# Performance work log

Hardware: AMD Instinct MI355X
Metric: run time of the kernel (lower is better)

## Reference

```python
import jax, jax.numpy as jnp
import numpy as np

SEQ = 4096
EMBED = 1280
HEADS = 16
HEAD_DIM = EMBED // HEADS  # 80


def rotate_half(x):
    # interleaved rotate: out[..., 2i] = -x[..., 2i+1]; out[..., 2i+1] = x[..., 2i]
    x_even = x[..., ::2]
    x_odd = x[..., 1::2]
    return jnp.stack((-x_odd, x_even), axis=-1).reshape(x.shape)


def setup_inputs() -> dict:
    key = jax.random.key(0)
    ks = jax.random.split(key, 7)
    return {
        "hidden_states": jax.random.normal(ks[0], (SEQ, EMBED), dtype=jnp.float32),
        "cos": jax.random.uniform(ks[1], (SEQ, HEAD_DIM), dtype=jnp.float32),
        "sin": jax.random.uniform(ks[2], (SEQ, HEAD_DIM), dtype=jnp.float32),
        "w_qkv": jax.random.normal(ks[3], (EMBED, 3 * EMBED), dtype=jnp.float32) * 0.02,
        "b_qkv": jax.random.normal(ks[4], (3 * EMBED,), dtype=jnp.float32) * 0.02,
        "w_proj": jax.random.normal(ks[5], (EMBED, EMBED), dtype=jnp.float32) * 0.02,
        "b_proj": jax.random.normal(ks[6], (EMBED,), dtype=jnp.float32) * 0.02,
    }


def reference(hidden_states, cos, sin, w_qkv, b_qkv, w_proj, b_proj):
    S = hidden_states.shape[0]
    # QKV projection: (S, 3E) -> (S, 3, H, D)
    qkv = (hidden_states @ w_qkv + b_qkv).reshape(S, 3, HEADS, HEAD_DIM)
    q, k, v = qkv[:, 0], qkv[:, 1], qkv[:, 2]  # each (S, H, D)

    # RoPE in float32, cos/sin broadcast over heads: (S, 1, D)
    dt = q.dtype
    qf, kf = q.astype(jnp.float32), k.astype(jnp.float32)
    c = cos[:, None, :].astype(jnp.float32)
    s = sin[:, None, :].astype(jnp.float32)
    q = (qf * c + rotate_half(qf) * s).astype(dt)
    k = (kf * c + rotate_half(kf) * s).astype(dt)

    scaling = HEAD_DIM ** -0.5
    # attention scores per head: (H, S, S)
    scores = jnp.einsum("shd,thd->hst", q, k) * scaling
    attn = jax.nn.softmax(scores.astype(jnp.float32), axis=-1).astype(dt)
    # weighted values: (S, H, D)
    out = jnp.einsum("hst,thd->shd", attn, v).reshape(S, EMBED)
    return out @ w_proj + b_proj
```

## Files before the change

### kernel.cpp

```cpp
#include <hip/hip_runtime.h>
#include <hip/hip_bf16.h>

#define SEQ   4096
#define EMBED 1280
#define NH    16
#define HD    80
#define K1    EMBED
#define N1    (3*EMBED)

typedef short bfrag_t __attribute__((ext_vector_type(8)));
typedef float f32x4   __attribute__((ext_vector_type(4)));
typedef float f32x16  __attribute__((ext_vector_type(16)));

static __device__ __forceinline__ unsigned short f2bf(float x){
    __hip_bfloat16 h = __float2bfloat16(x);
    return __builtin_bit_cast(unsigned short, h);
}
static __device__ __forceinline__ float bf2f(unsigned short u){
    unsigned int v = ((unsigned int)u) << 16;
    return __builtin_bit_cast(float, v);
}

static __device__ __forceinline__ unsigned int pack2bf(float a, float b){
    unsigned int ua = __builtin_bit_cast(unsigned int, a) + 0x8000u;
    unsigned int ub = __builtin_bit_cast(unsigned int, b) + 0x8000u;
#if __has_builtin(__builtin_amdgcn_perm)
    return __builtin_amdgcn_perm(ub, ua, 0x07060302u);
#else
    return (ua >> 16) | (ub & 0xFFFF0000u);
#endif
}

static __device__ __forceinline__ float fast_exp2(float x){
#if __has_builtin(__builtin_amdgcn_exp2f)
    return __builtin_amdgcn_exp2f(x);
#else
    return __expf(x * 0.69314718056f);
#endif
}

static __device__ __forceinline__ void gload_lds16(const void* g, void* l){
#if __has_builtin(__builtin_amdgcn_global_load_lds)
    __builtin_amdgcn_global_load_lds(
        (const __attribute__((address_space(1))) unsigned int*)g,
        (__attribute__((address_space(3))) unsigned int*)l, 16, 0, 0);
#else
    *(uint4*)l = *(const uint4*)g;
#endif
}


__global__ __launch_bounds__(256) void f32_to_bf16_k(const float* __restrict__ in,
                                                     unsigned short* __restrict__ out){
    int i = blockIdx.x * 256 + threadIdx.x;
    float4 v = ((const float4*)in)[i];
    ushort4 r;
    r.x = f2bf(v.x); r.y = f2bf(v.y); r.z = f2bf(v.z); r.w = f2bf(v.w);
    ((ushort4*)out)[i] = r;
}

__global__ __launch_bounds__(256) void transpose_to_bf16(const float* __restrict__ in,
                                                         unsigned short* __restrict__ out,
                                                         int R, int C){
    __shared__ float t[32][33];
    int bc = blockIdx.x * 32, br = blockIdx.y * 32;
    int tx = threadIdx.x & 31, ty = threadIdx.x >> 5;
    for (int i = ty; i < 32; i += 8) t[i][tx] = in[(size_t)(br + i) * C + bc + tx];
    __syncthreads();
    for (int i = ty; i < 32; i += 8) out[(size_t)(bc + i) * R + br + tx] = f2bf(t[tx][i]);
}


template<int EPI>
__global__ __launch_bounds__(256)
void gemm128(const unsigned short* __restrict__ A,
             const unsigned short* __restrict__ BT,
             const float* __restrict__ bias,
             const float* __restrict__ cosp, const float* __restrict__ sinp,
             unsigned short* __restrict__ qout, unsigned short* __restrict__ kout,
             unsigned short* __restrict__ vout,
             float* __restrict__ out,
             int M, int N, int K)
{
    __shared__ union {
        struct { unsigned short A[128*32]; unsigned short B[128*32]; } ab;
        unsigned short tr[4][64][72];
    } lds;

    int tid  = threadIdx.x;
    int lane = tid & 63, wave = tid >> 6;
    int wm = wave >> 1, wn = wave & 1;
    int quad = lane >> 4, l16 = lane & 15;
    int m0 = blockIdx.y * 128, n0 = blockIdx.x * 128;

    f32x4 acc[4][4] = {};
    const unsigned short* ga = A  + (size_t)(m0 + (tid>>2)) * K + (tid&3)*8;
    const unsigned short* gb = BT + (size_t)(n0 + (tid>>2)) * K + (tid&3)*8;

    for (int k0 = 0; k0 < K; k0 += 32){
        __syncthreads();
        gload_lds16(ga,                &lds.ab.A[tid*8]);
        gload_lds16(ga + (size_t)64*K, &lds.ab.A[2048 + tid*8]);
        gload_lds16(gb,                &lds.ab.B[tid*8]);
        gload_lds16(gb + (size_t)64*K, &lds.ab.B[2048 + tid*8]);
        ga += 32; gb += 32;
        __syncthreads();
        bfrag_t af[4], bf[4];
        #pragma unroll
        for (int i = 0; i < 4; i++)
            af[i] = *(const bfrag_t*)&lds.ab.A[(wm*64 + i*16 + l16)*32 + quad*8];
        #pragma unroll
        for (int j = 0; j < 4; j++)
            bf[j] = *(const bfrag_t*)&lds.ab.B[(wn*64 + j*16 + l16)*32 + quad*8];
        #pragma unroll
        for (int i = 0; i < 4; i++)
            #pragma unroll
            for (int j = 0; j < 4; j++)
                acc[i][j] = __builtin_amdgcn_mfma_f32_16x16x32_bf16(af[i], bf[j], acc[i][j], 0, 0, 0);
    }

    const float scaling = 0.11180339887498949f;

    if (EPI == 0 && n0 >= 2*EMBED){
        __syncthreads();
        #pragma unroll
        for (int j = 0; j < 4; j++){
            int colw = j*16 + l16;
            float b = bias[n0 + wn*64 + colw];
            #pragma unroll
            for (int i = 0; i < 4; i++){
                ushort4 u;
                u.x = f2bf(acc[i][j][0] + b);
                u.y = f2bf(acc[i][j][1] + b);
                u.z = f2bf(acc[i][j][2] + b);
                u.w = f2bf(acc[i][j][3] + b);
                *(ushort4*)&lds.tr[wave][colw][i*16 + quad*4] = u;
            }
        }
        int c8 = lane >> 3, rc = lane & 7;
        #pragma unroll
        for (int cg = 0; cg < 8; cg++){
            int colw = cg*8 + c8;
            size_t colg = (size_t)(n0 - 2*EMBED) + wn*64 + colw;
            int rowg = m0 + wm*64 + rc*8;
            *(uint4*)&vout[colg*SEQ + rowg] = *(const uint4*)&lds.tr[wave][colw][rc*8];
        }
        return;
    }

    #pragma unroll
    for (int i = 0; i < 4; i++)
    #pragma unroll
    for (int j = 0; j < 4; j++){
        int col = n0 + wn*64 + j*16 + l16;
        float b = bias[col];
        #pragma unroll
        for (int r = 0; r < 4; r++){
            int row = m0 + wm*64 + i*16 + quad*4 + r;
            float v = acc[i][j][r] + b;
            if (EPI == 0){
                int which = col / EMBED;
                int rem   = col % EMBED;
                int h = rem / HD, d = rem % HD;
                float vo = __shfl_xor(v, 1, 64);
                float c = cosp[(size_t)row*HD + d];
                float s = sinp[(size_t)row*HD + d];
                float o = (d & 1) ? (v*c + vo*s) : (v*c - vo*s);
                if (which == 0)
                    qout[((size_t)h*SEQ + row)*HD + d] = f2bf(o * scaling);
                else
                    kout[((size_t)h*SEQ + row)*HD + d] = f2bf(o);
            } else {
                out[(size_t)row * N + col] = v;
            }
        }
    }
}


__global__ __launch_bounds__(256, 4)
void attn_mfma(const unsigned short* __restrict__ q,
               const unsigned short* __restrict__ k,
               const unsigned short* __restrict__ vt,
               unsigned short* __restrict__ out,
               unsigned short* __restrict__ opart,
               float* __restrict__ lpart,
               int iters)
{
    __shared__ unsigned short Vt[2][80*64];
    __shared__ unsigned short Ps[128][72];

    int tid  = threadIdx.x;
    int lane = tid & 63, wave = tid >> 6;
    int quad = lane >> 4, l16 = lane & 15;
    int l32  = lane & 31, h2 = lane >> 5;
    int h = blockIdx.y, q0 = blockIdx.x * 128;
    int split = blockIdx.z;
    int kb0 = split * iters * 64;
    int qrow = wave*32 + l32;

    const unsigned short* qh = q  + ((size_t)h*SEQ + q0)*HD;
    const unsigned short* kh = k  + (size_t)h*SEQ*HD;
    const unsigned short* vh = vt + (size_t)h*HD*SEQ;

    bfrag_t qf[5];
    #pragma unroll
    for (int kk = 0; kk < 5; kk++)
        qf[kk] = *(const bfrag_t*)&qh[(size_t)qrow*HD + (kk*2 + h2)*8];

    auto stage = [&](int buf, int kb){
        unsigned short* dst = &Vt[buf][0];
        #pragma unroll
        for (int rnd = 0; rnd < 3; rnd++){
            int idx = rnd*256 + tid;
            if (rnd < 2 || tid < 128){
                int row = idx >> 3, c = idx & 7;
                gload_lds16(&vh[(size_t)row*SEQ + kb + ((c ^ (row & 7)) << 3)], &dst[idx*8]);
            }
        }
    };

    stage(0, kb0);

    float la = 0.f, lb = 0.f;
    f32x4 o_[2][5] = {};

    const unsigned short* kp0 = kh + (size_t)(kb0 + l32)*HD + h2*8;
    const unsigned short* kp1 = kp0 + (size_t)32*HD;
    const float LOG2E = 1.44269504f;
    const float BIAS2 = -17.3123405f;

    for (int kt = 0; kt < iters; kt++){
        f32x16 S0 = {}, S1 = {};
        #pragma unroll
        for (int kk = 0; kk < 5; kk++){
            bfrag_t kf0 = *(const bfrag_t*)(kp0 + kk*16);
            bfrag_t kf1 = *(const bfrag_t*)(kp1 + kk*16);
            S0 = __builtin_amdgcn_mfma_f32_32x32x16_bf16(kf0, qf[kk], S0, 0,0,0);
            S1 = __builtin_amdgcn_mfma_f32_32x32x16_bf16(kf1, qf[kk], S1, 0,0,0);
        }
        kp0 += (size_t)64*HD; kp1 += (size_t)64*HD;

        #pragma unroll
        for (int r = 0; r < 16; r++){
            float p0 = fast_exp2(fmaf(S0[r], LOG2E, BIAS2));
            float p1 = fast_exp2(fmaf(S1[r], LOG2E, BIAS2));
            S0[r] = p0; S1[r] = p1;
            la += p0; lb += p1;
        }

        unsigned int* prow = (unsigned int*)&Ps[qrow][h2*4];
        #pragma unroll
        for (int g = 0; g < 4; g++){
            uint2 w0, w1;
            w0.x = pack2bf(S0[g*4+0], S0[g*4+1]);
            w0.y = pack2bf(S0[g*4+2], S0[g*4+3]);
            w1.x = pack2bf(S1[g*4+0], S1[g*4+1]);
            w1.y = pack2bf(S1[g*4+2], S1[g*4+3]);
            *(uint2*)&prow[g*4]      = w0;
            *(uint2*)&prow[16 + g*4] = w1;
        }

        __syncthreads();
        if (kt < iters - 1) stage((kt+1)&1, kb0 + (kt+1)*64);

        int buf = kt & 1;
        #pragma unroll
        for (int kk = 0; kk < 2; kk++){
            bfrag_t pf0 = *(const bfrag_t*)&Ps[wave*32      + l16][(kk*4+quad)*8];
            bfrag_t pf1 = *(const bfrag_t*)&Ps[wave*32 + 16 + l16][(kk*4+quad)*8];
            #pragma unroll
            for (int dt = 0; dt < 5; dt++){
                int row = dt*16 + l16;
                bfrag_t vf = *(const bfrag_t*)&Vt[buf][row*64 + (((kk*4+quad) ^ (l16 & 7)) << 3)];
                o_[0][dt] = __builtin_amdgcn_mfma_f32_16x16x32_bf16(vf, pf0, o_[0][dt], 0,0,0);
                o_[1][dt] = __builtin_amdgcn_mfma_f32_16x16x32_bf16(vf, pf1, o_[1][dt], 0,0,0);
            }
        }
    }

    float l_ = la + lb;
    l_ += __shfl_xor(l_, 32, 64);

    if (gridDim.z == 1){
        #pragma unroll
        for (int i = 0; i < 2; i++){
            float linv = 1.f / __shfl(l_, i*16 + l16, 64);
            int qg = q0 + wave*32 + i*16 + l16;
            #pragma unroll
            for (int dt = 0; dt < 5; dt++){
                int d = dt*16 + quad*4;
                ushort4 u;
                u.x = f2bf(o_[i][dt][0]*linv);
                u.y = f2bf(o_[i][dt][1]*linv);
                u.z = f2bf(o_[i][dt][2]*linv);
                u.w = f2bf(o_[i][dt][3]*linv);
                *(ushort4*)&out[(size_t)qg*EMBED + h*HD + d] = u;
            }
        }
    } else {
        if (h2 == 0)
            lpart[((size_t)(split*NH + h))*SEQ + q0 + qrow] = l_;
        #pragma unroll
        for (int i = 0; i < 2; i++){
            int qg = q0 + wave*32 + i*16 + l16;
            size_t base = (((size_t)(split*NH + h))*SEQ + qg)*HD;
            #pragma unroll
            for (int dt = 0; dt < 5; dt++){
                int d = dt*16 + quad*4;
                ushort4 u;
                u.x = f2bf(o_[i][dt][0]);
                u.y = f2bf(o_[i][dt][1]);
                u.z = f2bf(o_[i][dt][2]);
                u.w = f2bf(o_[i][dt][3]);
                *(ushort4*)&opart[base + d] = u;
            }
        }
    }
}

__global__ __launch_bounds__(256)
void attn_combine(const unsigned short* __restrict__ op,
                  const float* __restrict__ lp,
                  unsigned short* __restrict__ out)
{
    int t = blockIdx.x*256 + threadIdx.x;
    int d8 = t % 10;
    int qh = t / 10;
    int q  = qh & (SEQ-1);
    int h  = qh >> 12;
    size_t b0 = (((size_t)h*SEQ) + q)*HD + d8*8;
    size_t b1 = (((size_t)(NH + h)*SEQ) + q)*HD + d8*8;
    float inv = 1.f / (lp[(size_t)h*SEQ + q] + lp[(size_t)(NH + h)*SEQ + q]);
    uint4 A = *(const uint4*)&op[b0];
    uint4 B = *(const uint4*)&op[b1];
    uint4 R;
    unsigned int* a = (unsigned int*)&A;
    unsigned int* b = (unsigned int*)&B;
    unsigned int* r = (unsigned int*)&R;
    #pragma unroll
    for (int e = 0; e < 4; e++){
        float lo = (bf2f((unsigned short)(a[e] & 0xffff)) + bf2f((unsigned short)(b[e] & 0xffff))) * inv;
        float hi = (bf2f((unsigned short)(a[e] >> 16))    + bf2f((unsigned short)(b[e] >> 16)))    * inv;
        r[e] = pack2bf(lo, hi);
    }
    *(uint4*)&out[(size_t)q*EMBED + h*HD + d8*8] = R;
}


extern "C" void kernel_launch(void* const* d_in, const int* in_sizes, int n_in,
                              void* d_out, int out_size, void* d_ws, size_t ws_size,
                              hipStream_t stream)
{
    const float* hs    = (const float*)d_in[0];
    const float* cosp  = (const float*)d_in[1];
    const float* sinp  = (const float*)d_in[2];
    const float* wqkv  = (const float*)d_in[3];
    const float* bqkv  = (const float*)d_in[4];
    const float* wproj = (const float*)d_in[5];
    const float* bproj = (const float*)d_in[6];
    float* out = (float*)d_out;

    char* ws = (char*)d_ws;
    size_t off = 0;
    auto alloc = [&](size_t bytes){ void* p = ws + off; off += bytes; return p; };
    unsigned short* hb    = (unsigned short*)alloc((size_t)SEQ*EMBED*2);
    unsigned short* wqT   = (unsigned short*)alloc((size_t)N1*K1*2);
    unsigned short* wpT   = (unsigned short*)alloc((size_t)EMBED*EMBED*2);
    unsigned short* q_ws  = (unsigned short*)alloc((size_t)SEQ*EMBED*2);
    unsigned short* k_ws  = (unsigned short*)alloc((size_t)SEQ*EMBED*2);
    unsigned short* v_ws  = (unsigned short*)alloc((size_t)SEQ*EMBED*2);
    unsigned short* a_ws  = (unsigned short*)alloc((size_t)SEQ*EMBED*2);
    unsigned short* opart = (unsigned short*)alloc((size_t)2*NH*SEQ*HD*2);
    float*          lpart = (float*)alloc((size_t)2*NH*SEQ*4);
    int nsplit = (ws_size >= off) ? 2 : 1;

    f32_to_bf16_k<<<SEQ*EMBED/4/256, 256, 0, stream>>>(hs, hb);
    transpose_to_bf16<<<dim3(N1/32,    K1/32),    256, 0, stream>>>(wqkv,  wqT, K1,    N1);
    transpose_to_bf16<<<dim3(EMBED/32, EMBED/32), 256, 0, stream>>>(wproj, wpT, EMBED, EMBED);

    gemm128<0><<<dim3(N1/128, SEQ/128), 256, 0, stream>>>(
        hb, wqT, bqkv, cosp, sinp, q_ws, k_ws, v_ws, nullptr, SEQ, N1, K1);

    attn_mfma<<<dim3(SEQ/128, NH, nsplit), 256, 0, stream>>>(
        q_ws, k_ws, v_ws, a_ws, opart, lpart, (SEQ/64)/nsplit);
    if (nsplit == 2)
        attn_combine<<<NH*SEQ*10/256, 256, 0, stream>>>(opart, lpart, a_ws);

    gemm128<1><<<dim3(EMBED/128, SEQ/128), 256, 0, stream>>>(
        a_ws, wpT, bproj, nullptr, nullptr, nullptr, nullptr, nullptr, out, SEQ, EMBED, EMBED);
}
```

Baseline: 337.6 us.

## Prefetch K fragments into registers and restage RoPE epilogue through LDS

The attention loop now loads the next tile's K fragments into registers while the current QK^T MFMAs and softmax run. The V tile staging moves to the end of each iteration behind a single barrier at the top, instead of a mid-loop barrier. The P scratch buffer is repadded to 68 columns and read with two 8-byte loads per fragment. The QKV GEMM RoPE epilogue writes float results into an LDS tile, then emits coalesced 4-element bf16 stores instead of scattered 2-byte stores. The K prefetch raises register pressure, which may hurt occupancy at the 4-blocks-per-SIMD launch bound.

```diff
diff --git a/kernel.cpp b/kernel.cpp
--- a/kernel.cpp
+++ b/kernel.cpp
@@ -47,6 +47,13 @@
 #else
     *(uint4*)l = *(const uint4*)g;
 #endif
+}
+
+static __device__ __forceinline__ bfrag_t ld_frag8(const unsigned short* p){
+    uint2 lo = *(const uint2*)p;
+    uint2 hi = *(const uint2*)(p + 4);
+    uint4 u; u.x = lo.x; u.y = lo.y; u.z = hi.x; u.w = hi.y;
+    return __builtin_bit_cast(bfrag_t, u);
 }
 
 
@@ -85,6 +92,7 @@
     __shared__ union {
         struct { unsigned short A[128*32]; unsigned short B[128*32]; } ab;
         unsigned short tr[4][64][72];
+        float trf[4][16][68];
     } lds;
 
     int tid  = threadIdx.x;
@@ -148,6 +156,47 @@
         return;
     }
 
+    if (EPI == 0){
+        bool isq = (n0 < EMBED);
+        unsigned short* dst = isq ? qout : kout;
+        float mult = isq ? scaling : 1.f;
+        int colbase = (n0 - (isq ? 0 : EMBED)) + wn*64;
+        __syncthreads();
+        int rw = lane >> 2, cc = lane & 3;
+        #pragma unroll
+        for (int i = 0; i < 4; i++){
+            #pragma unroll
+            for (int j = 0; j < 4; j++){
+                int colw = j*16 + l16;
+                int col  = colbase + colw;
+                int d    = col % HD;
+                float b  = bias[n0 + wn*64 + colw];
+                #pragma unroll
+                for (int r = 0; r < 4; r++){
+                    int row = m0 + wm*64 + i*16 + quad*4 + r;
+                    float v = acc[i][j][r] + b;
+                    float vo = __shfl_xor(v, 1, 64);
+                    float c = cosp[(size_t)row*HD + d];
+                    float s = sinp[(size_t)row*HD + d];
+                    float o = (d & 1) ? (v*c + vo*s) : (v*c - vo*s);
+                    lds.trf[wave][quad*4 + r][colw] = o * mult;
+                }
+            }
+            #pragma unroll
+            for (int rnd = 0; rnd < 4; rnd++){
+                int colw = rnd*16 + cc*4;
+                float4 fv = *(const float4*)&lds.trf[wave][rw][colw];
+                int col = colbase + colw;
+                int hh = col / HD, d = col - hh*HD;
+                int rowg = m0 + wm*64 + i*16 + rw;
+                ushort4 u;
+                u.x = f2bf(fv.x); u.y = f2bf(fv.y); u.z = f2bf(fv.z); u.w = f2bf(fv.w);
+                *(ushort4*)&dst[((size_t)hh*SEQ + rowg)*HD + d] = u;
+            }
+        }
+        return;
+    }
+
     #pragma unroll
     for (int i = 0; i < 4; i++)
     #pragma unroll
@@ -157,22 +206,7 @@
         #pragma unroll
         for (int r = 0; r < 4; r++){
             int row = m0 + wm*64 + i*16 + quad*4 + r;
-            float v = acc[i][j][r] + b;
-            if (EPI == 0){
-                int which = col / EMBED;
-                int rem   = col % EMBED;
-                int h = rem / HD, d = rem % HD;
-                float vo = __shfl_xor(v, 1, 64);
-                float c = cosp[(size_t)row*HD + d];
-                float s = sinp[(size_t)row*HD + d];
-                float o = (d & 1) ? (v*c + vo*s) : (v*c - vo*s);
-                if (which == 0)
-                    qout[((size_t)h*SEQ + row)*HD + d] = f2bf(o * scaling);
-                else
-                    kout[((size_t)h*SEQ + row)*HD + d] = f2bf(o);
-            } else {
-                out[(size_t)row * N + col] = v;
-            }
+            out[(size_t)row * N + col] = acc[i][j][r] + b;
         }
     }
 }
@@ -188,7 +222,7 @@
                int iters)
 {
     __shared__ unsigned short Vt[2][80*64];
-    __shared__ unsigned short Ps[128][72];
+    __shared__ unsigned short Ps[128][68];
 
     int tid  = threadIdx.x;
     int lane = tid & 63, wave = tid >> 6;
@@ -225,21 +259,36 @@
     float la = 0.f, lb = 0.f;
     f32x4 o_[2][5] = {};
 
-    const unsigned short* kp0 = kh + (size_t)(kb0 + l32)*HD + h2*8;
-    const unsigned short* kp1 = kp0 + (size_t)32*HD;
+    const unsigned short* kp = kh + (size_t)(kb0 + l32)*HD + h2*8;
     const float LOG2E = 1.44269504f;
     const float BIAS2 = -17.3123405f;
 
+    bfrag_t kf[10];
+    #pragma unroll
+    for (int kk = 0; kk < 5; kk++){
+        kf[kk]   = *(const bfrag_t*)(kp + kk*16);
+        kf[5+kk] = *(const bfrag_t*)(kp + (size_t)32*HD + kk*16);
+    }
+    kp += (size_t)64*HD;
+
     for (int kt = 0; kt < iters; kt++){
+        __syncthreads();
+
         f32x16 S0 = {}, S1 = {};
         #pragma unroll
         for (int kk = 0; kk < 5; kk++){
-            bfrag_t kf0 = *(const bfrag_t*)(kp0 + kk*16);
-            bfrag_t kf1 = *(const bfrag_t*)(kp1 + kk*16);
-            S0 = __builtin_amdgcn_mfma_f32_32x32x16_bf16(kf0, qf[kk], S0, 0,0,0);
-            S1 = __builtin_amdgcn_mfma_f32_32x32x16_bf16(kf1, qf[kk], S1, 0,0,0);
-        }
-        kp0 += (size_t)64*HD; kp1 += (size_t)64*HD;
+            S0 = __builtin_amdgcn_mfma_f32_32x32x16_bf16(kf[kk],   qf[kk], S0, 0,0,0);
+            S1 = __builtin_amdgcn_mfma_f32_32x32x16_bf16(kf[5+kk], qf[kk], S1, 0,0,0);
+        }
+
+        if (kt + 1 < iters){
+            #pragma unroll
+            for (int kk = 0; kk < 5; kk++){
+                kf[kk]   = *(const bfrag_t*)(kp + kk*16);
+                kf[5+kk] = *(const bfrag_t*)(kp + (size_t)32*HD + kk*16);
+            }
+            kp += (size_t)64*HD;
+        }
 
         #pragma unroll
         for (int r = 0; r < 16; r++){
@@ -249,7 +298,6 @@
             la += p0; lb += p1;
         }
 
-        unsigned int* prow = (unsigned int*)&Ps[qrow][h2*4];
         #pragma unroll
         for (int g = 0; g < 4; g++){
             uint2 w0, w1;
@@ -257,18 +305,15 @@
             w0.y = pack2bf(S0[g*4+2], S0[g*4+3]);
             w1.x = pack2bf(S1[g*4+0], S1[g*4+1]);
             w1.y = pack2bf(S1[g*4+2], S1[g*4+3]);
-            *(uint2*)&prow[g*4]      = w0;
-            *(uint2*)&prow[16 + g*4] = w1;
-        }
-
-        __syncthreads();
-        if (kt < iters - 1) stage((kt+1)&1, kb0 + (kt+1)*64);
+            *(uint2*)&Ps[qrow][g*8 + h2*4]      = w0;
+            *(uint2*)&Ps[qrow][32 + g*8 + h2*4] = w1;
+        }
 
         int buf = kt & 1;
         #pragma unroll
         for (int kk = 0; kk < 2; kk++){
-            bfrag_t pf0 = *(const bfrag_t*)&Ps[wave*32      + l16][(kk*4+quad)*8];
-            bfrag_t pf1 = *(const bfrag_t*)&Ps[wave*32 + 16 + l16][(kk*4+quad)*8];
+            bfrag_t pf0 = ld_frag8(&Ps[wave*32      + l16][kk*32 + quad*8]);
+            bfrag_t pf1 = ld_frag8(&Ps[wave*32 + 16 + l16][kk*32 + quad*8]);
             #pragma unroll
             for (int dt = 0; dt < 5; dt++){
                 int row = dt*16 + l16;
@@ -277,6 +322,8 @@
                 o_[1][dt] = __builtin_amdgcn_mfma_f32_16x16x32_bf16(vf, pf1, o_[1][dt], 0,0,0);
             }
         }
+
+        if (kt + 1 < iters) stage((kt+1)&1, kb0 + (kt+1)*64);
     }
 
     float l_ = la + lb;
```

Measured after the change: 1.031 ms. +205.3%, slower.

## Software-pipeline attention loop: defer PV to next iteration, prefetch K, repack P tile

Applied to the files above, without the earlier changes.

Restructures the attention main loop so the P·V MFMAs for tile kt-1 run at the top of iteration kt, interleaved with the K fragment loads for tile kt. The single barrier now precedes the QK^T of the current tile instead of sitting between P writes and PV reads, and the final PV is done after the loop. K fragments are loaded in full register arrays ahead of use, and the P scratch row stride drops from 72 to 68 with a reordered column layout, read back with two 8-byte loads. The aim is to hide global and LDS latency and cut bank conflicts, at the cost of more live registers and possible occupancy pressure.

```diff
diff --git a/kernel.cpp b/kernel.cpp
--- a/kernel.cpp
+++ b/kernel.cpp
@@ -47,6 +47,13 @@
 #else
     *(uint4*)l = *(const uint4*)g;
 #endif
+}
+
+static __device__ __forceinline__ bfrag_t ld_frag8(const unsigned short* p){
+    uint2 lo = *(const uint2*)p;
+    uint2 hi = *(const uint2*)(p + 4);
+    uint4 u; u.x = lo.x; u.y = lo.y; u.z = hi.x; u.w = hi.y;
+    return __builtin_bit_cast(bfrag_t, u);
 }
 
 
@@ -188,7 +195,7 @@
                int iters)
 {
     __shared__ unsigned short Vt[2][80*64];
-    __shared__ unsigned short Ps[128][72];
+    __shared__ unsigned short Ps[128][68];
 
     int tid  = threadIdx.x;
     int lane = tid & 63, wave = tid >> 6;
@@ -220,26 +227,59 @@
         }
     };
 
+    auto pv = [&](int buf, f32x4 (&o_)[2][5]){
+        #pragma unroll
+        for (int kk = 0; kk < 2; kk++){
+            bfrag_t pf0 = ld_frag8(&Ps[wave*32      + l16][kk*32 + quad*8]);
+            bfrag_t pf1 = ld_frag8(&Ps[wave*32 + 16 + l16][kk*32 + quad*8]);
+            #pragma unroll
+            for (int dt = 0; dt < 5; dt++){
+                int row = dt*16 + l16;
+                bfrag_t vf = *(const bfrag_t*)&Vt[buf][row*64 + (((kk*4+quad) ^ (l16 & 7)) << 3)];
+                o_[0][dt] = __builtin_amdgcn_mfma_f32_16x16x32_bf16(vf, pf0, o_[0][dt], 0,0,0);
+                o_[1][dt] = __builtin_amdgcn_mfma_f32_16x16x32_bf16(vf, pf1, o_[1][dt], 0,0,0);
+            }
+        }
+    };
+
     stage(0, kb0);
 
     float la = 0.f, lb = 0.f;
     f32x4 o_[2][5] = {};
 
-    const unsigned short* kp0 = kh + (size_t)(kb0 + l32)*HD + h2*8;
-    const unsigned short* kp1 = kp0 + (size_t)32*HD;
+    const unsigned short* kp = kh + (size_t)(kb0 + l32)*HD + h2*8;
     const float LOG2E = 1.44269504f;
     const float BIAS2 = -17.3123405f;
 
+    bfrag_t kf0[5];
+    #pragma unroll
+    for (int kk = 0; kk < 5; kk++)
+        kf0[kk] = *(const bfrag_t*)(kp + kk*16);
+
     for (int kt = 0; kt < iters; kt++){
+        if (kt > 0){
+            #pragma unroll
+            for (int kk = 0; kk < 5; kk++)
+                kf0[kk] = *(const bfrag_t*)(kp + kk*16);
+            pv((kt-1)&1, o_);
+        }
+
+        __syncthreads();
+
+        if (kt + 1 < iters) stage((kt+1)&1, kb0 + (kt+1)*64);
+
+        bfrag_t kf1[5];
+        #pragma unroll
+        for (int kk = 0; kk < 5; kk++)
+            kf1[kk] = *(const bfrag_t*)(kp + (size_t)32*HD + kk*16);
         f32x16 S0 = {}, S1 = {};
         #pragma unroll
-        for (int kk = 0; kk < 5; kk++){
-            bfrag_t kf0 = *(const bfrag_t*)(kp0 + kk*16);
-            bfrag_t kf1 = *(const bfrag_t*)(kp1 + kk*16);
-            S0 = __builtin_amdgcn_mfma_f32_32x32x16_bf16(kf0, qf[kk], S0, 0,0,0);
-            S1 = __builtin_amdgcn_mfma_f32_32x32x16_bf16(kf1, qf[kk], S1, 0,0,0);
-        }
-        kp0 += (size_t)64*HD; kp1 += (size_t)64*HD;
+        for (int kk = 0; kk < 5; kk++)
+            S0 = __builtin_amdgcn_mfma_f32_32x32x16_bf16(kf0[kk], qf[kk], S0, 0,0,0);
+        #pragma unroll
+        for (int kk = 0; kk < 5; kk++)
+            S1 = __builtin_amdgcn_mfma_f32_32x32x16_bf16(kf1[kk], qf[kk], S1, 0,0,0);
+        kp += (size_t)64*HD;
 
         #pragma unroll
         for (int r = 0; r < 16; r++){
@@ -249,7 +289,6 @@
             la += p0; lb += p1;
         }
 
-        unsigned int* prow = (unsigned int*)&Ps[qrow][h2*4];
         #pragma unroll
         for (int g = 0; g < 4; g++){
             uint2 w0, w1;
@@ -257,27 +296,12 @@
             w0.y = pack2bf(S0[g*4+2], S0[g*4+3]);
             w1.x = pack2bf(S1[g*4+0], S1[g*4+1]);
             w1.y = pack2bf(S1[g*4+2], S1[g*4+3]);
-            *(uint2*)&prow[g*4]      = w0;
-            *(uint2*)&prow[16 + g*4] = w1;
-        }
-
-        __syncthreads();
-        if (kt < iters - 1) stage((kt+1)&1, kb0 + (kt+1)*64);
-
-        int buf = kt & 1;
-        #pragma unroll
-        for (int kk = 0; kk < 2; kk++){
-            bfrag_t pf0 = *(const bfrag_t*)&Ps[wave*32      + l16][(kk*4+quad)*8];
-            bfrag_t pf1 = *(const bfrag_t*)&Ps[wave*32 + 16 + l16][(kk*4+quad)*8];
-            #pragma unroll
-            for (int dt = 0; dt < 5; dt++){
-                int row = dt*16 + l16;
-                bfrag_t vf = *(const bfrag_t*)&Vt[buf][row*64 + (((kk*4+quad) ^ (l16 & 7)) << 3)];
-                o_[0][dt] = __builtin_amdgcn_mfma_f32_16x16x32_bf16(vf, pf0, o_[0][dt], 0,0,0);
-                o_[1][dt] = __builtin_amdgcn_mfma_f32_16x16x32_bf16(vf, pf1, o_[1][dt], 0,0,0);
-            }
-        }
-    }
+            *(uint2*)&Ps[qrow][g*8 + h2*4]      = w0;
+            *(uint2*)&Ps[qrow][32 + g*8 + h2*4] = w1;
+        }
+    }
+
+    pv((iters-1)&1, o_);
 
     float l_ = la + lb;
     l_ += __shfl_xor(l_, 32, 64);
```

Measured after the change: 339.4 us. No clear change (+0.6%).
